# Optimization experiments

Hardware: AMD Instinct MI355X
Metric: run time of the kernel (lower is better)

The kernel has to match this reference:

```python
import jax, jax.numpy as jnp
import numpy as np

H, C = 2, 16          # heads, per-head channels (hidden_dim//2)
HD = H * C            # 32 = hidden_dim (concat heads)
NEG_SLOPE = 0.2       # PyG GATConv default negative_slope


def _gat(x, src, dst, edge_attr, lin_w, att_src, att_dst, edge_w, att_edge, bias):
    # Faithful PyG GATConv(in, C, heads=H, edge_dim=2, concat=True) in eval mode
    # (dropout inactive). add_self_loops=True with fill_value='mean' for edge_attr.
    N = x.shape[0]
    ones = jnp.ones((src.shape[0],), x.dtype)
    cnt = jax.ops.segment_sum(ones, dst, num_segments=N)
    mean_attr = jax.ops.segment_sum(edge_attr, dst, num_segments=N) / jnp.maximum(cnt, 1.0)[:, None]
    loop = jnp.arange(N, dtype=src.dtype)
    src_a = jnp.concatenate([src, loop])
    dst_a = jnp.concatenate([dst, loop])
    ea = jnp.concatenate([edge_attr, mean_attr], axis=0)            # [E+N, 2]
    xp = (x @ lin_w).reshape(N, H, C)                               # [N,H,C]
    a_src = (xp * att_src).sum(-1)                                  # [N,H]
    a_dst = (xp * att_dst).sum(-1)                                  # [N,H]
    ee = (ea @ edge_w).reshape(-1, H, C)                            # [E+N,H,C]
    a_edge = (ee * att_edge).sum(-1)                                # [E+N,H]
    alpha = jax.nn.leaky_relu(a_src[src_a] + a_dst[dst_a] + a_edge, NEG_SLOPE)
    m = jax.ops.segment_max(alpha, dst_a, num_segments=N)           # segment softmax over dst
    alpha = jnp.exp(alpha - m[dst_a])
    denom = jax.ops.segment_sum(alpha, dst_a, num_segments=N)
    alpha = alpha / (denom[dst_a] + 1e-16)
    msg = xp[src_a] * alpha[:, :, None]                             # [E+N,H,C]
    out = jax.ops.segment_sum(msg, dst_a, num_segments=N).reshape(N, HD)
    return out + bias


def _forward(group_ids, ord_feats, edge_index, edge_attr, pool_rows, pool_cols,
             pool_vals, P, embedding, g1, g2, g3, head_w1, head_b1, head_w2, head_b2):
    src, dst = edge_index[0], edge_index[1]
    x = jnp.concatenate([embedding[group_ids], ord_feats], axis=1)  # [N,20]
    h = jax.nn.relu(_gat(x, src, dst, edge_attr, *g1))
    h = jax.nn.relu(_gat(h, src, dst, edge_attr, *g2))
    h = jax.nn.relu(_gat(h, src, dst, edge_attr, *g3))              # [N,32]
    # sparse (P,N) Gaussian pooling matmul, COO form
    pooled = jax.ops.segment_sum(pool_vals[:, None] * h[pool_cols], pool_rows, num_segments=P)
    hh = jax.nn.relu(pooled @ head_w1 + head_b1)
    return (hh @ head_w2 + head_b2)[:, 0]                           # [P]


def setup_inputs() -> dict:
    key = jax.random.key(0)
    ks = jax.random.split(key, 32)
    N, E, P, NNZ, G = 100000, 3200000, 200000, 3200000, 19
    def nrm(k, shape, s=0.1):
        return jax.random.normal(k, shape, dtype=jnp.float32) * s
    inp = dict(
        group_ids=jax.random.randint(ks[0], (N,), 0, G, dtype=jnp.int32),
        ord_feats=jax.random.uniform(ks[1], (N, 4), dtype=jnp.float32),
        edge_index=jax.random.randint(ks[2], (2, E), 0, N, dtype=jnp.int32),
        edge_attr=jax.random.uniform(ks[3], (E, 2), dtype=jnp.float32),
        pool_rows=jax.random.randint(ks[4], (NNZ,), 0, P, dtype=jnp.int32),
        pool_cols=jax.random.randint(ks[5], (NNZ,), 0, N, dtype=jnp.int32),
        pool_vals=jax.random.uniform(ks[6], (NNZ,), dtype=jnp.float32),
        P=P,
        embedding=nrm(ks[7], (G, 16)),
    )
    ind = [20, HD, HD]
    for li in range(3):
        b = 8 + li * 6
        inp[f"g{li+1}_lin_w"] = nrm(ks[b], (ind[li], HD), (2.0 / (ind[li] + HD)) ** 0.5)
        inp[f"g{li+1}_att_src"] = nrm(ks[b + 1], (H, C))
        inp[f"g{li+1}_att_dst"] = nrm(ks[b + 2], (H, C))
        inp[f"g{li+1}_edge_w"] = nrm(ks[b + 3], (2, HD), 0.5)
        inp[f"g{li+1}_att_edge"] = nrm(ks[b + 4], (H, C))
        inp[f"g{li+1}_bias"] = jnp.zeros((HD,), jnp.float32)
    inp["head_w1"] = nrm(ks[26], (HD, 32), (2.0 / 64) ** 0.5)
    inp["head_b1"] = jnp.zeros((32,), jnp.float32)
    inp["head_w2"] = nrm(ks[27], (32, 1), (2.0 / 33) ** 0.5)
    inp["head_b2"] = jnp.zeros((1,), jnp.float32)
    return inp


def reference(group_ids, ord_feats, edge_index, edge_attr, pool_rows, pool_cols, pool_vals, P,
              embedding,
              g1_lin_w, g1_att_src, g1_att_dst, g1_edge_w, g1_att_edge, g1_bias,
              g2_lin_w, g2_att_src, g2_att_dst, g2_edge_w, g2_att_edge, g2_bias,
              g3_lin_w, g3_att_src, g3_att_dst, g3_edge_w, g3_att_edge, g3_bias,
              head_w1, head_b1, head_w2, head_b2):
    g1 = (g1_lin_w, g1_att_src, g1_att_dst, g1_edge_w, g1_att_edge, g1_bias)
    g2 = (g2_lin_w, g2_att_src, g2_att_dst, g2_edge_w, g2_att_edge, g2_bias)
    g3 = (g3_lin_w, g3_att_src, g3_att_dst, g3_edge_w, g3_att_edge, g3_bias)
    return _forward(group_ids, ord_feats, edge_index, edge_attr, pool_rows, pool_cols,
                    pool_vals, P, embedding, g1, g2, g3, head_w1, head_b1, head_w2, head_b2)
```

## Files before the change

kernel.cpp:

```cpp
#include <hip/hip_runtime.h>
#include <hip/hip_fp16.h>

#define TPB 256
#define STPB 1024
#define TILE 8192

__device__ __forceinline__ float leaky02(float x){ return x > 0.f ? x : 0.2f*x; }
__device__ __forceinline__ unsigned pack_h2(float a, float b){
  return (unsigned)__half_as_ushort(__float2half_rn(a)) |
         ((unsigned)__half_as_ushort(__float2half_rn(b)) << 16);
}

__global__ void k_scan_tile(const int* __restrict__ in, int* __restrict__ out,
                            int* __restrict__ bsum, int n) {
  __shared__ int sh[TPB];
  int t = threadIdx.x;
  int base = blockIdx.x * (TPB*4) + t*4;
  int v0=0,v1=0,v2=0,v3=0;
  if (base+0 < n) v0 = in[base+0];
  if (base+1 < n) v1 = in[base+1];
  if (base+2 < n) v2 = in[base+2];
  if (base+3 < n) v3 = in[base+3];
  int tsum = v0+v1+v2+v3;
  sh[t] = tsum; __syncthreads();
  for (int off=1; off<TPB; off<<=1){
    int x = (t>=off) ? sh[t-off] : 0;
    __syncthreads();
    sh[t] += x;
    __syncthreads();
  }
  int incl = sh[t];
  int excl = incl - tsum;
  if (t == TPB-1) bsum[blockIdx.x] = incl;
  int run = excl;
  if (base+0 < n){ out[base+0] = run; run += v0; }
  if (base+1 < n){ out[base+1] = run; run += v1; }
  if (base+2 < n){ out[base+2] = run; run += v2; }
  if (base+3 < n){ out[base+3] = run; run += v3; }
}

__global__ void k_scan_small(int* __restrict__ a, int n) {
  __shared__ int sh[TPB];
  __shared__ int carry;
  int t = threadIdx.x;
  if (t==0) carry = 0;
  __syncthreads();
  for (int base=0; base<n; base+=TPB){
    int v = (base+t < n) ? a[base+t] : 0;
    sh[t] = v; __syncthreads();
    for (int off=1; off<TPB; off<<=1){
      int x = (t>=off)? sh[t-off]:0; __syncthreads();
      sh[t]+=x; __syncthreads();
    }
    int c0 = carry;
    if (base+t < n) a[base+t] = c0 + sh[t] - v;
    int tot = sh[TPB-1];
    __syncthreads();
    if (t==0) carry = c0 + tot;
    __syncthreads();
  }
}

__global__ void k_scan_add(int* __restrict__ out, const int* __restrict__ bsum,
                           int n, int total) {
  int i = blockIdx.x*TPB + threadIdx.x;
  if (i < n) out[i] += bsum[i >> 10];
  if (i == 0) out[n] = total;
}

__global__ __launch_bounds__(STPB) void k_split_hist(
    const int* __restrict__ key, int n, int shift, int T,
    int* __restrict__ hist, int nbc){
  __shared__ int cnt[512];
  int b = blockIdx.x, t = threadIdx.x;
  for (int k=t;k<nbc;k+=STPB) cnt[k]=0;
  __syncthreads();
  int i0 = b*TILE, end = min(n, i0+TILE);
  for (int i=i0+t; i<end; i+=STPB) atomicAdd(&cnt[key[i]>>shift], 1);
  __syncthreads();
  for (int k=t;k<nbc;k+=STPB) hist[(size_t)k*T + b] = cnt[k];
}

__global__ __launch_bounds__(STPB) void k_split_scatter_edges(
    const int* __restrict__ src, const int* __restrict__ dst,
    const float* __restrict__ eattr, int E, int T,
    const int* __restrict__ hist, int2* __restrict__ tmp, int nbc){
  __shared__ int nxt[512];
  int b = blockIdx.x, t = threadIdx.x;
  for (int k=t;k<nbc;k+=STPB) nxt[k] = hist[(size_t)k*T + b];
  __syncthreads();
  int i0 = b*TILE, end = min(E, i0+TILE);
  for (int i=i0+t; i<end; i+=STPB){
    int d = dst[i];
    int k = d>>8;
    int pos = atomicAdd(&nxt[k], 1);
    float2 ea = ((const float2*)eattr)[i];
    tmp[pos] = make_int2(src[i] | ((d & 255)<<17), (int)pack_h2(ea.x, ea.y));
  }
}

__global__ __launch_bounds__(STPB) void k_split_scatter_pool(
    const int* __restrict__ rows, const int* __restrict__ cols,
    const float* __restrict__ vals, int n, int T,
    const int* __restrict__ hist, int2* __restrict__ tmp, int nbc){
  __shared__ int nxt[512];
  int b = blockIdx.x, t = threadIdx.x;
  for (int k=t;k<nbc;k+=STPB) nxt[k] = hist[(size_t)k*T + b];
  __syncthreads();
  int i0 = b*TILE, end = min(n, i0+TILE);
  for (int i=i0+t; i<end; i+=STPB){
    int r = rows[i];
    int k = r>>9;
    int pos = atomicAdd(&nxt[k], 1);
    tmp[pos] = make_int2(cols[i] | ((r & 511)<<17), __float_as_int(vals[i]));
  }
}

__global__ __launch_bounds__(STPB) void k_finalize_edges(
    const int2* __restrict__ tmp, const int* __restrict__ hist, int T, int E,
    int N, int* __restrict__ rs, int2* __restrict__ rec){
  __shared__ int cnt[256];
  __shared__ int sh[256];
  int b = blockIdx.x, t = threadIdx.x;
  int base = hist[(size_t)b*T];
  int endv = (b+1 < (int)gridDim.x) ? hist[(size_t)(b+1)*T] : E;
  int size = endv - base;
  if (t < 256) cnt[t] = 0;
  __syncthreads();
  for (int i=t; i<size; i+=STPB) atomicAdd(&cnt[(((unsigned)tmp[base+i].x)>>17)&255], 1);
  __syncthreads();
  int v = 0;
  if (t < 256){ v = cnt[t]; sh[t] = v; }
  __syncthreads();
  for (int off=1; off<256; off<<=1){
    int x = 0;
    if (t < 256 && t >= off) x = sh[t-off];
    __syncthreads();
    if (t < 256) sh[t] += x;
    __syncthreads();
  }
  if (t < 256){
    int excl = sh[t] - v;
    int d = (b<<8)+t;
    if (d<=N) rs[d] = base + excl;
    cnt[t] = excl;
  }
  __syncthreads();
  for (int i=t; i<size; i+=STPB){
    int2 q = tmp[base+i];
    int k = (((unsigned)q.x)>>17)&255;
    int p = atomicAdd(&cnt[k],1);
    rec[base+p] = make_int2(q.x & 0x1FFFF, q.y);
  }
}

__global__ __launch_bounds__(TPB) void k_mattr(
    const int2* __restrict__ rec, const int* __restrict__ rs,
    float2* __restrict__ mattr, int N){
  int n = blockIdx.x*(TPB/4) + (threadIdx.x>>2);
  if (n >= N) return;
  int l4 = threadIdx.x & 3;
  int jb = rs[n], je = rs[n+1];
  float sx = 0.f, sy = 0.f;
  for (int j = jb + l4; j < je; j += 4){
    float2 ea = __half22float2(*(const __half2*)&rec[j].y);
    sx += ea.x; sy += ea.y;
  }
  sx += __shfl_xor(sx, 1); sx += __shfl_xor(sx, 2);
  sy += __shfl_xor(sy, 1); sy += __shfl_xor(sy, 2);
  if (l4 == 0){
    int cn = je - jb;
    float inv = 1.0f/(float)(cn > 0 ? cn : 1);
    mattr[n] = make_float2(sx*inv, sy*inv);
  }
}

__global__ __launch_bounds__(STPB) void k_finalize_pool(
    const int2* __restrict__ tmp, const int* __restrict__ hist, int T, int NNZ,
    int P, int* __restrict__ rs, int2* __restrict__ rec){
  __shared__ int cnt[512];
  __shared__ int sh[256];
  __shared__ int carry_s;
  int b = blockIdx.x, t = threadIdx.x;
  int base = hist[(size_t)b*T];
  int endv = (b+1 < (int)gridDim.x) ? hist[(size_t)(b+1)*T] : NNZ;
  int size = endv - base;
  if (t < 512) cnt[t] = 0;
  __syncthreads();
  for (int i=t;i<size;i+=STPB) atomicAdd(&cnt[(((unsigned)tmp[base+i].x)>>17)&511], 1);
  __syncthreads();
  int excl0 = 0, excl1 = 0;
  int v0 = 0;
  if (t < 256){ v0 = cnt[t]; sh[t] = v0; }
  __syncthreads();
  for (int off=1; off<256; off<<=1){
    int x = 0;
    if (t < 256 && t >= off) x = sh[t-off];
    __syncthreads();
    if (t < 256) sh[t] += x;
    __syncthreads();
  }
  if (t < 256) excl0 = sh[t] - v0;
  if (t == 255) carry_s = sh[255];
  __syncthreads();
  int v1 = 0;
  if (t < 256){ v1 = cnt[256+t]; sh[t] = v1; }
  __syncthreads();
  for (int off=1; off<256; off<<=1){
    int x = 0;
    if (t < 256 && t >= off) x = sh[t-off];
    __syncthreads();
    if (t < 256) sh[t] += x;
    __syncthreads();
  }
  if (t < 256) excl1 = carry_s + sh[t] - v1;
  __syncthreads();
  if (t < 256){
    cnt[t] = excl0; cnt[256+t] = excl1;
    int r0 = (b<<9)+t;
    if (r0<=P) rs[r0] = base+excl0;
    int r1 = r0+256;
    if (r1<=P) rs[r1] = base+excl1;
  }
  __syncthreads();
  for (int i=t;i<size;i+=STPB){
    int2 q = tmp[base+i];
    int k = (((unsigned)q.x)>>17)&511;
    int p = atomicAdd(&cnt[k],1);
    rec[base+p] = make_int2(q.x & 0x1FFFF, q.y);
  }
}

__global__ void k_weff(const float* __restrict__ ew1, const float* __restrict__ ae1,
                       const float* __restrict__ ew2, const float* __restrict__ ae2,
                       const float* __restrict__ ew3, const float* __restrict__ ae3,
                       float* __restrict__ weff){
  int t = threadIdx.x;
  if (t >= 6) return;
  int l = t>>1, h = t&1;
  const float* ew = l==0?ew1:(l==1?ew2:ew3);
  const float* ae = l==0?ae1:(l==1?ae2:ae3);
  float w0=0.f, w1=0.f;
  for (int c=0;c<16;c++){
    float a = ae[h*16+c];
    w0 += ew[h*16+c]*a;
    w1 += ew[32+h*16+c]*a;
  }
  weff[l*4+h*2]   = w0;
  weff[l*4+h*2+1] = w1;
}

__global__ __launch_bounds__(TPB) void k_node_pre1(
    const int* __restrict__ gid, const float* __restrict__ ord, const float* __restrict__ emb,
    const float* __restrict__ lin_w, const float* __restrict__ att_src, const float* __restrict__ att_dst,
    __half* __restrict__ xp16, float* __restrict__ asrc, float* __restrict__ adst, int N){
  __shared__ float W[20*32];
  __shared__ float As[32], Ad[32];
  for (int i=threadIdx.x; i<20*32; i+=TPB) W[i]=lin_w[i];
  if (threadIdx.x < 32){ As[threadIdx.x]=att_src[threadIdx.x]; Ad[threadIdx.x]=att_dst[threadIdx.x]; }
  __syncthreads();
  int n = blockIdx.x*TPB+threadIdx.x;
  if (n>=N) return;
  float x[20];
  int g = gid[n];
  #pragma unroll
  for (int k=0;k<16;k++) x[k]=emb[g*16+k];
  float4 o4 = ((const float4*)ord)[n];
  x[16]=o4.x; x[17]=o4.y; x[18]=o4.z; x[19]=o4.w;
  float acc[32];
  #pragma unroll
  for (int c=0;c<32;c++) acc[c]=0.f;
  #pragma unroll
  for (int k=0;k<20;k++){
    float xk=x[k];
    #pragma unroll
    for (int c=0;c<32;c++) acc[c] += xk*W[k*32+c];
  }
  float s0=0,s1=0,d0=0,d1=0;
  #pragma unroll
  for (int c=0;c<16;c++){
    s0+=acc[c]*As[c];      d0+=acc[c]*Ad[c];
    s1+=acc[16+c]*As[16+c]; d1+=acc[16+c]*Ad[16+c];
  }
  unsigned us[16];
  #pragma unroll
  for (int k=0;k<16;k++) us[k] = pack_h2(acc[2*k], acc[2*k+1]);
  uint4* o = (uint4*)(xp16 + (size_t)n*32);
  o[0]=make_uint4(us[0],us[1],us[2],us[3]);
  o[1]=make_uint4(us[4],us[5],us[6],us[7]);
  o[2]=make_uint4(us[8],us[9],us[10],us[11]);
  o[3]=make_uint4(us[12],us[13],us[14],us[15]);
  asrc[2*n]=s0; asrc[2*n+1]=s1; adst[2*n]=d0; adst[2*n+1]=d1;
}

__global__ __launch_bounds__(TPB) void k_node_pre(
    const float* __restrict__ hin,
    const float* __restrict__ lin_w, const float* __restrict__ att_src, const float* __restrict__ att_dst,
    __half* __restrict__ xp16, float* __restrict__ asrc, float* __restrict__ adst, int N){
  __shared__ float W[32*32];
  __shared__ float As[32], Ad[32];
  for (int i=threadIdx.x; i<1024; i+=TPB) W[i]=lin_w[i];
  if (threadIdx.x < 32){ As[threadIdx.x]=att_src[threadIdx.x]; Ad[threadIdx.x]=att_dst[threadIdx.x]; }
  __syncthreads();
  int n = blockIdx.x*TPB+threadIdx.x;
  if (n>=N) return;
  float x[32];
  const float4* hi = (const float4*)(hin + (size_t)n*32);
  #pragma unroll
  for (int q=0;q<8;q++){ float4 v=hi[q]; x[4*q]=v.x; x[4*q+1]=v.y; x[4*q+2]=v.z; x[4*q+3]=v.w; }
  float acc[32];
  #pragma unroll
  for (int c=0;c<32;c++) acc[c]=0.f;
  #pragma unroll
  for (int k=0;k<32;k++){
    float xk=x[k];
    #pragma unroll
    for (int c=0;c<32;c++) acc[c] += xk*W[k*32+c];
  }
  float s0=0,s1=0,d0=0,d1=0;
  #pragma unroll
  for (int c=0;c<16;c++){
    s0+=acc[c]*As[c];       d0+=acc[c]*Ad[c];
    s1+=acc[16+c]*As[16+c]; d1+=acc[16+c]*Ad[16+c];
  }
  unsigned us[16];
  #pragma unroll
  for (int k=0;k<16;k++) us[k] = pack_h2(acc[2*k], acc[2*k+1]);
  uint4* o = (uint4*)(xp16 + (size_t)n*32);
  o[0]=make_uint4(us[0],us[1],us[2],us[3]);
  o[1]=make_uint4(us[4],us[5],us[6],us[7]);
  o[2]=make_uint4(us[8],us[9],us[10],us[11]);
  o[3]=make_uint4(us[12],us[13],us[14],us[15]);
  asrc[2*n]=s0; asrc[2*n+1]=s1; adst[2*n]=d0; adst[2*n+1]=d1;
}

__global__ __launch_bounds__(TPB) void k_agg(
    const __half* __restrict__ xp16, const float* __restrict__ asrc, const float* __restrict__ adst,
    const int* __restrict__ rs, const int2* __restrict__ rec,
    const float2* __restrict__ mattr,
    const float* __restrict__ weff_l,
    const float* __restrict__ bias, float* __restrict__ houtf, __half* __restrict__ hout16, int N)
{
  int lane = threadIdx.x & 63;
  int node_slot = lane >> 4;
  int n = blockIdx.x*16 + (threadIdx.x>>6)*4 + node_slot;
  if (n >= N) return;
  int sub = (lane >> 2) & 3;
  int l4  = lane & 3;
  int h   = l4 >> 1;
  float2 wv = ((const float2*)weff_l)[h];
  float adn = adst[2*n+h];
  float ax0=0,ay0=0,ax1=0,ay1=0,ax2=0,ay2=0,ax3=0,ay3=0;
  float den=0.f;
  int jb = rs[n], je = rs[n+1];
  int j = jb + sub;
  for (; j + 4 < je; j += 8){
    int2 r1 = rec[j];
    int2 r2 = rec[j+4];
    uint4 u1 = ((const uint4*)(xp16 + (size_t)r1.x*32))[l4];
    uint4 u2 = ((const uint4*)(xp16 + (size_t)r2.x*32))[l4];
    float as1 = asrc[2*r1.x+h];
    float as2 = asrc[2*r2.x+h];
    float2 e1 = __half22float2(*(const __half2*)&r1.y);
    float2 e2 = __half22float2(*(const __half2*)&r2.y);
    float p1 = __expf(leaky02(as1 + adn + e1.x*wv.x + e1.y*wv.y));
    float p2 = __expf(leaky02(as2 + adn + e2.x*wv.x + e2.y*wv.y));
    float2 f;
    f=__half22float2(*(const __half2*)&u1.x); ax0+=p1*f.x; ay0+=p1*f.y;
    f=__half22float2(*(const __half2*)&u1.y); ax1+=p1*f.x; ay1+=p1*f.y;
    f=__half22float2(*(const __half2*)&u1.z); ax2+=p1*f.x; ay2+=p1*f.y;
    f=__half22float2(*(const __half2*)&u1.w); ax3+=p1*f.x; ay3+=p1*f.y;
    f=__half22float2(*(const __half2*)&u2.x); ax0+=p2*f.x; ay0+=p2*f.y;
    f=__half22float2(*(const __half2*)&u2.y); ax1+=p2*f.x; ay1+=p2*f.y;
    f=__half22float2(*(const __half2*)&u2.z); ax2+=p2*f.x; ay2+=p2*f.y;
    f=__half22float2(*(const __half2*)&u2.w); ax3+=p2*f.x; ay3+=p2*f.y;
    den += p1 + p2;
  }
  if (j < je){
    int2 r1 = rec[j];
    uint4 u1 = ((const uint4*)(xp16 + (size_t)r1.x*32))[l4];
    float as1 = asrc[2*r1.x+h];
    float2 e1 = __half22float2(*(const __half2*)&r1.y);
    float p1 = __expf(leaky02(as1 + adn + e1.x*wv.x + e1.y*wv.y));
    float2 f;
    f=__half22float2(*(const __half2*)&u1.x); ax0+=p1*f.x; ay0+=p1*f.y;
    f=__half22float2(*(const __half2*)&u1.y); ax1+=p1*f.x; ay1+=p1*f.y;
    f=__half22float2(*(const __half2*)&u1.z); ax2+=p1*f.x; ay2+=p1*f.y;
    f=__half22float2(*(const __half2*)&u1.w); ax3+=p1*f.x; ay3+=p1*f.y;
    den += p1;
  }
  #pragma unroll
  for (int m=4; m<16; m<<=1){
    ax0+=__shfl_xor(ax0,m); ay0+=__shfl_xor(ay0,m);
    ax1+=__shfl_xor(ax1,m); ay1+=__shfl_xor(ay1,m);
    ax2+=__shfl_xor(ax2,m); ay2+=__shfl_xor(ay2,m);
    ax3+=__shfl_xor(ax3,m); ay3+=__shfl_xor(ay3,m);
    den+=__shfl_xor(den,m);
  }
  if (sub == 0){
    float2 ma = mattr[n];
    float al = leaky02(asrc[2*n+h] + adn + ma.x*wv.x + ma.y*wv.y);
    float p = __expf(al);
    uint4 u = ((const uint4*)(xp16 + (size_t)n*32))[l4];
    float2 f0 = __half22float2(*(const __half2*)&u.x);
    float2 f1 = __half22float2(*(const __half2*)&u.y);
    float2 f2 = __half22float2(*(const __half2*)&u.z);
    float2 f3 = __half22float2(*(const __half2*)&u.w);
    ax0 += p*f0.x; ay0 += p*f0.y;
    ax1 += p*f1.x; ay1 += p*f1.y;
    ax2 += p*f2.x; ay2 += p*f2.y;
    ax3 += p*f3.x; ay3 += p*f3.y;
    den += p;
    float dinv = 1.0f/(den + 1e-16f);
    float4 b0 = ((const float4*)bias)[l4*2];
    float4 b1 = ((const float4*)bias)[l4*2+1];
    float o0 = fmaxf(ax0*dinv + b0.x, 0.f);
    float o1 = fmaxf(ay0*dinv + b0.y, 0.f);
    float o2 = fmaxf(ax1*dinv + b0.z, 0.f);
    float o3 = fmaxf(ay1*dinv + b0.w, 0.f);
    float o4 = fmaxf(ax2*dinv + b1.x, 0.f);
    float o5 = fmaxf(ay2*dinv + b1.y, 0.f);
    float o6 = fmaxf(ax3*dinv + b1.z, 0.f);
    float o7 = fmaxf(ay3*dinv + b1.w, 0.f);
    if (houtf){
      float4* o = (float4*)(houtf + (size_t)n*32);
      o[l4*2]   = make_float4(o0,o1,o2,o3);
      o[l4*2+1] = make_float4(o4,o5,o6,o7);
    }
    if (hout16){
      ((uint4*)(hout16 + (size_t)n*32))[l4] =
        make_uint4(pack_h2(o0,o1), pack_h2(o2,o3), pack_h2(o4,o5), pack_h2(o6,o7));
    }
  }
}

__global__ __launch_bounds__(TPB) void k_pool_q(
    const __half* __restrict__ h3, const int* __restrict__ rsP,
    const int2* __restrict__ rec, float* __restrict__ pooled, int P){
  int p = blockIdx.x*(TPB/4) + (threadIdx.x>>2);
  if (p >= P) return;
  int l4 = threadIdx.x & 3;
  float ax0=0,ay0=0,ax1=0,ay1=0,ax2=0,ay2=0,ax3=0,ay3=0;
  int jb = rsP[p], je = rsP[p+1];
  int j = jb;
  for (; j+3 < je; j += 4){
    int2 q1 = rec[j];
    int2 q2 = rec[j+1];
    int2 q3 = rec[j+2];
    int2 q4 = rec[j+3];
    uint4 u1 = ((const uint4*)(h3 + (size_t)q1.x*32))[l4];
    uint4 u2 = ((const uint4*)(h3 + (size_t)q2.x*32))[l4];
    uint4 u3 = ((const uint4*)(h3 + (size_t)q3.x*32))[l4];
    uint4 u4 = ((const uint4*)(h3 + (size_t)q4.x*32))[l4];
    float v1 = __int_as_float(q1.y);
    float v2 = __int_as_float(q2.y);
    float v3 = __int_as_float(q3.y);
    float v4 = __int_as_float(q4.y);
    float2 f;
    f=__half22float2(*(const __half2*)&u1.x); ax0+=v1*f.x; ay0+=v1*f.y;
    f=__half22float2(*(const __half2*)&u1.y); ax1+=v1*f.x; ay1+=v1*f.y;
    f=__half22float2(*(const __half2*)&u1.z); ax2+=v1*f.x; ay2+=v1*f.y;
    f=__half22float2(*(const __half2*)&u1.w); ax3+=v1*f.x; ay3+=v1*f.y;
    f=__half22float2(*(const __half2*)&u2.x); ax0+=v2*f.x; ay0+=v2*f.y;
    f=__half22float2(*(const __half2*)&u2.y); ax1+=v2*f.x; ay1+=v2*f.y;
    f=__half22float2(*(const __half2*)&u2.z); ax2+=v2*f.x; ay2+=v2*f.y;
    f=__half22float2(*(const __half2*)&u2.w); ax3+=v2*f.x; ay3+=v2*f.y;
    f=__half22float2(*(const __half2*)&u3.x); ax0+=v3*f.x; ay0+=v3*f.y;
    f=__half22float2(*(const __half2*)&u3.y); ax1+=v3*f.x; ay1+=v3*f.y;
    f=__half22float2(*(const __half2*)&u3.z); ax2+=v3*f.x; ay2+=v3*f.y;
    f=__half22float2(*(const __half2*)&u3.w); ax3+=v3*f.x; ay3+=v3*f.y;
    f=__half22float2(*(const __half2*)&u4.x); ax0+=v4*f.x; ay0+=v4*f.y;
    f=__half22float2(*(const __half2*)&u4.y); ax1+=v4*f.x; ay1+=v4*f.y;
    f=__half22float2(*(const __half2*)&u4.z); ax2+=v4*f.x; ay2+=v4*f.y;
    f=__half22float2(*(const __half2*)&u4.w); ax3+=v4*f.x; ay3+=v4*f.y;
  }
  for (; j < je; ++j){
    int2 q1 = rec[j];
    uint4 u1 = ((const uint4*)(h3 + (size_t)q1.x*32))[l4];
    float v1 = __int_as_float(q1.y);
    float2 f;
    f=__half22float2(*(const __half2*)&u1.x); ax0+=v1*f.x; ay0+=v1*f.y;
    f=__half22float2(*(const __half2*)&u1.y); ax1+=v1*f.x; ay1+=v1*f.y;
    f=__half22float2(*(const __half2*)&u1.z); ax2+=v1*f.x; ay2+=v1*f.y;
    f=__half22float2(*(const __half2*)&u1.w); ax3+=v1*f.x; ay3+=v1*f.y;
  }
  float4* o = (float4*)(pooled + (size_t)p*32);
  o[l4*2]   = make_float4(ax0,ay0,ax1,ay1);
  o[l4*2+1] = make_float4(ax2,ay2,ax3,ay3);
}

__global__ __launch_bounds__(TPB) void k_head(
    const float* __restrict__ pooled,
    const float* __restrict__ W1, const float* __restrict__ b1,
    const float* __restrict__ W2, const float* __restrict__ b2,
    float* __restrict__ out, int P){
  __shared__ float sW1[32*32];
  __shared__ float sb1[32], sW2[32];
  for (int i=threadIdx.x;i<1024;i+=TPB) sW1[i]=W1[i];
  if (threadIdx.x<32){ sb1[threadIdx.x]=b1[threadIdx.x]; sW2[threadIdx.x]=W2[threadIdx.x]; }
  __syncthreads();
  int p = blockIdx.x*TPB + threadIdx.x;
  if (p >= P) return;
  float x[32];
  const float4* pi = (const float4*)(pooled + (size_t)p*32);
  #pragma unroll
  for (int q=0;q<8;q++){ float4 v=pi[q]; x[4*q]=v.x; x[4*q+1]=v.y; x[4*q+2]=v.z; x[4*q+3]=v.w; }
  float r = 0.f;
  #pragma unroll
  for (int c=0;c<32;c++){
    float hh = sb1[c];
    #pragma unroll
    for (int k=0;k<32;k++) hh += x[k]*sW1[k*32+c];
    r += fmaxf(hh, 0.f) * sW2[c];
  }
  out[p] = r + b2[0];
}

extern "C" void kernel_launch(void* const* d_in, const int* in_sizes, int n_in,
                              void* d_out, int out_size, void* d_ws, size_t ws_size,
                              hipStream_t stream){
  const int*   group_ids = (const int*)d_in[0];
  const float* ord       = (const float*)d_in[1];
  const int*   eidx      = (const int*)d_in[2];
  const float* eattr     = (const float*)d_in[3];
  const int*   prow      = (const int*)d_in[4];
  const int*   pcol      = (const int*)d_in[5];
  const float* pval      = (const float*)d_in[6];
  const float* emb       = (const float*)d_in[8];
  const float* head_w1   = (const float*)d_in[27];
  const float* head_b1   = (const float*)d_in[28];
  const float* head_w2   = (const float*)d_in[29];
  const float* head_b2   = (const float*)d_in[30];

  int N   = in_sizes[0];
  int E   = in_sizes[2]/2;
  int NNZ = in_sizes[4];
  int P   = out_size;

  const int* src = eidx;
  const int* dst = eidx + E;

  int NBC_E = (N+255)>>8;
  int T_E   = (E + TILE-1)/TILE;
  int nHistE = NBC_E*T_E;
  int NBC_P = (P+511)>>9;
  int T_P   = (NNZ + TILE-1)/TILE;
  int nHistP = NBC_P*T_P;
  int nHistMax = nHistE > nHistP ? nHistE : nHistP;
  size_t recMax = (size_t)(E > NNZ ? E : NNZ);

  char* w = (char*)d_ws;
  auto alloc = [&](size_t bytes)->char*{ char* p=w; w += (bytes+255)&~255ull; return p; };
  int*    hist = (int*)   alloc(4ull*(nHistMax+16));
  int*    bsum = (int*)   alloc(4ull*4096);
  int*    rs   = (int*)   alloc(4ull*(N+1));
  int*    rsP  = (int*)   alloc(4ull*(P+1));
  int2*   rec  = (int2*)  alloc(8ull*recMax);
  int2*   tmp  = (int2*)  alloc(8ull*recMax);
  __half* xp16 = (__half*)alloc(2ull*32*N);
  float*  asrc = (float*) alloc(8ull*N);
  float*  adst = (float*) alloc(8ull*N);
  float*  hbuf = (float*) alloc(4ull*32*N);
  float*  weff = (float*) alloc(256);
  float2* mattr= (float2*)alloc(8ull*N);
  __half* h316 = (__half*)hbuf;
  float*  pooled = (float*)tmp;

  int gN = (N+TPB-1)/TPB;

  k_split_hist<<<T_E,STPB,0,stream>>>(dst, E, 8, T_E, hist, NBC_E);
  int nbE = (nHistE+1023)/1024;
  k_scan_tile<<<nbE,TPB,0,stream>>>(hist, hist, bsum, nHistE);
  k_scan_small<<<1,TPB,0,stream>>>(bsum, nbE);
  k_scan_add<<<(nHistE+TPB-1)/TPB,TPB,0,stream>>>(hist, bsum, nHistE, E);
  k_split_scatter_edges<<<T_E,STPB,0,stream>>>(src, dst, eattr, E, T_E, hist, tmp, NBC_E);
  k_finalize_edges<<<NBC_E,STPB,0,stream>>>(tmp, hist, T_E, E, N, rs, rec);
  int gmt = (N + TPB/4 - 1)/(TPB/4);
  k_mattr<<<gmt,TPB,0,stream>>>(rec, rs, mattr, N);

  k_weff<<<1,64,0,stream>>>((const float*)d_in[12], (const float*)d_in[13],
                            (const float*)d_in[18], (const float*)d_in[19],
                            (const float*)d_in[24], (const float*)d_in[25], weff);

  k_node_pre1<<<gN,TPB,0,stream>>>(group_ids, ord, emb,
      (const float*)d_in[9], (const float*)d_in[10], (const float*)d_in[11],
      xp16, asrc, adst, N);
  int gagg = (N+15)/16;
  k_agg<<<gagg,TPB,0,stream>>>(xp16, asrc, adst, rs, rec, mattr, weff+0,
      (const float*)d_in[14], hbuf, (__half*)nullptr, N);
  k_node_pre<<<gN,TPB,0,stream>>>(hbuf,
      (const float*)d_in[15], (const float*)d_in[16], (const float*)d_in[17],
      xp16, asrc, adst, N);
  k_agg<<<gagg,TPB,0,stream>>>(xp16, asrc, adst, rs, rec, mattr, weff+4,
      (const float*)d_in[20], hbuf, (__half*)nullptr, N);
  k_node_pre<<<gN,TPB,0,stream>>>(hbuf,
      (const float*)d_in[21], (const float*)d_in[22], (const float*)d_in[23],
      xp16, asrc, adst, N);
  k_agg<<<gagg,TPB,0,stream>>>(xp16, asrc, adst, rs, rec, mattr, weff+8,
      (const float*)d_in[26], (float*)nullptr, h316, N);

  k_split_hist<<<T_P,STPB,0,stream>>>(prow, NNZ, 9, T_P, hist, NBC_P);
  int nbP = (nHistP+1023)/1024;
  k_scan_tile<<<nbP,TPB,0,stream>>>(hist, hist, bsum, nHistP);
  k_scan_small<<<1,TPB,0,stream>>>(bsum, nbP);
  k_scan_add<<<(nHistP+TPB-1)/TPB,TPB,0,stream>>>(hist, bsum, nHistP, NNZ);
  k_split_scatter_pool<<<T_P,STPB,0,stream>>>(prow, pcol, pval, NNZ, T_P, hist, tmp, NBC_P);
  k_finalize_pool<<<NBC_P,STPB,0,stream>>>(tmp, hist, T_P, NNZ, P, rsP, rec);

  int gpq = (P + TPB/4 - 1)/(TPB/4);
  k_pool_q<<<gpq,TPB,0,stream>>>(h316, rsP, rec, pooled, P);
  k_head<<<(P+TPB-1)/TPB,TPB,0,stream>>>(pooled,
      head_w1, head_b1, head_w2, head_b2, (float*)d_out, P);
}
```

Before: 414.5 us.

## Stage radix-split scatter through LDS for coalesced bucket writes

The edge and pool split-scatter kernels now build a local histogram and prefix scan per tile, place records into an LDS buffer grouped by bucket, then copy each bucket contiguously to global memory one wave at a time. This replaces random scattered 8-byte global stores with mostly coalesced runs. In exchange each block recounts its keys, runs two 256-wide scans with many barriers, and uses 64KB of LDS, which limits occupancy to about one block per CU.

```diff
diff --git a/kernel.cpp b/kernel.cpp
--- a/kernel.cpp
+++ b/kernel.cpp
@@ -85,17 +85,62 @@
     const int* __restrict__ src, const int* __restrict__ dst,
     const float* __restrict__ eattr, int E, int T,
     const int* __restrict__ hist, int2* __restrict__ tmp, int nbc){
-  __shared__ int nxt[512];
+  __shared__ int lcur[512];
+  __shared__ int lbase[512];
+  __shared__ int gbase[512];
+  __shared__ int sh[256];
+  __shared__ int carry_s;
+  __shared__ int2 buf[TILE];
   int b = blockIdx.x, t = threadIdx.x;
-  for (int k=t;k<nbc;k+=STPB) nxt[k] = hist[(size_t)k*T + b];
+  for (int k=t;k<512;k+=STPB) lcur[k]=0;
   __syncthreads();
   int i0 = b*TILE, end = min(E, i0+TILE);
+  for (int i=i0+t; i<end; i+=STPB) atomicAdd(&lcur[dst[i]>>8], 1);
+  __syncthreads();
+  int v0 = 0;
+  if (t < 256){ v0 = lcur[t]; sh[t] = v0; }
+  __syncthreads();
+  for (int off=1; off<256; off<<=1){
+    int x = 0;
+    if (t < 256 && t >= off) x = sh[t-off];
+    __syncthreads();
+    if (t < 256) sh[t] += x;
+    __syncthreads();
+  }
+  if (t < 256) lbase[t] = sh[t] - v0;
+  if (t == 255) carry_s = sh[255];
+  __syncthreads();
+  int v1 = 0;
+  if (t < 256){ v1 = lcur[256+t]; sh[t] = v1; }
+  __syncthreads();
+  for (int off=1; off<256; off<<=1){
+    int x = 0;
+    if (t < 256 && t >= off) x = sh[t-off];
+    __syncthreads();
+    if (t < 256) sh[t] += x;
+    __syncthreads();
+  }
+  if (t < 256) lbase[256+t] = carry_s + sh[t] - v1;
+  __syncthreads();
+  if (t < 512){
+    lcur[t] = lbase[t];
+    gbase[t] = (t < nbc) ? hist[(size_t)t*T + b] : 0;
+  }
+  __syncthreads();
   for (int i=i0+t; i<end; i+=STPB){
     int d = dst[i];
     int k = d>>8;
-    int pos = atomicAdd(&nxt[k], 1);
+    int pos = atomicAdd(&lcur[k], 1);
     float2 ea = ((const float2*)eattr)[i];
-    tmp[pos] = make_int2(src[i] | ((d & 255)<<17), (int)pack_h2(ea.x, ea.y));
+    buf[pos] = make_int2(src[i] | ((d & 255)<<17), (int)pack_h2(ea.x, ea.y));
+  }
+  __syncthreads();
+  int wave = t >> 6, lane = t & 63;
+  for (int k=wave; k<nbc; k+=STPB/64){
+    int s = lbase[k];
+    int c = lcur[k] - s;
+    int g = gbase[k];
+    for (int i=lane; i<c; i+=64) tmp[g+i] = buf[s+i];
   }
 }
 
@@ -103,16 +148,61 @@
     const int* __restrict__ rows, const int* __restrict__ cols,
     const float* __restrict__ vals, int n, int T,
     const int* __restrict__ hist, int2* __restrict__ tmp, int nbc){
-  __shared__ int nxt[512];
+  __shared__ int lcur[512];
+  __shared__ int lbase[512];
+  __shared__ int gbase[512];
+  __shared__ int sh[256];
+  __shared__ int carry_s;
+  __shared__ int2 buf[TILE];
   int b = blockIdx.x, t = threadIdx.x;
-  for (int k=t;k<nbc;k+=STPB) nxt[k] = hist[(size_t)k*T + b];
+  for (int k=t;k<512;k+=STPB) lcur[k]=0;
   __syncthreads();
   int i0 = b*TILE, end = min(n, i0+TILE);
+  for (int i=i0+t; i<end; i+=STPB) atomicAdd(&lcur[rows[i]>>9], 1);
+  __syncthreads();
+  int v0 = 0;
+  if (t < 256){ v0 = lcur[t]; sh[t] = v0; }
+  __syncthreads();
+  for (int off=1; off<256; off<<=1){
+    int x = 0;
+    if (t < 256 && t >= off) x = sh[t-off];
+    __syncthreads();
+    if (t < 256) sh[t] += x;
+    __syncthreads();
+  }
+  if (t < 256) lbase[t] = sh[t] - v0;
+  if (t == 255) carry_s = sh[255];
+  __syncthreads();
+  int v1 = 0;
+  if (t < 256){ v1 = lcur[256+t]; sh[t] = v1; }
+  __syncthreads();
+  for (int off=1; off<256; off<<=1){
+    int x = 0;
+    if (t < 256 && t >= off) x = sh[t-off];
+    __syncthreads();
+    if (t < 256) sh[t] += x;
+    __syncthreads();
+  }
+  if (t < 256) lbase[256+t] = carry_s + sh[t] - v1;
+  __syncthreads();
+  if (t < 512){
+    lcur[t] = lbase[t];
+    gbase[t] = (t < nbc) ? hist[(size_t)t*T + b] : 0;
+  }
+  __syncthreads();
   for (int i=i0+t; i<end; i+=STPB){
     int r = rows[i];
     int k = r>>9;
-    int pos = atomicAdd(&nxt[k], 1);
-    tmp[pos] = make_int2(cols[i] | ((r & 511)<<17), __float_as_int(vals[i]));
+    int pos = atomicAdd(&lcur[k], 1);
+    buf[pos] = make_int2(cols[i] | ((r & 511)<<17), __float_as_int(vals[i]));
+  }
+  __syncthreads();
+  int wave = t >> 6, lane = t & 63;
+  for (int k=wave; k<nbc; k+=STPB/64){
+    int s = lbase[k];
+    int c = lcur[k] - s;
+    int g = gbase[k];
+    for (int i=lane; i<c; i+=64) tmp[g+i] = buf[s+i];
   }
 }
 
```

Result: faster. 400.7 us (-3.3%).
